# Optimization experiments

Measured on AMD Instinct MI355X. Metric: run time of the kernel, lower is better.

## Reference

```python
import jax, jax.numpy as jnp
import numpy as np

N, D, H, P, B = 6000, 256, 8, 128, 16
DH = D // H


def _layernorm(x, g, b, eps=1e-5):
    mu = jnp.mean(x, axis=-1, keepdims=True)
    var = jnp.mean((x - mu) ** 2, axis=-1, keepdims=True)
    return (x - mu) * jax.lax.rsqrt(var + eps) * g + b


def setup_inputs() -> dict:
    key = jax.random.key(0)
    ks = jax.random.split(key, 12)
    s = 1.0 / np.sqrt(D)
    inp = {
        "H_genes": jax.random.normal(ks[0], (N, D), jnp.float32),
        "perturbation_indices": jax.random.randint(ks[1], (P,), 0, N),
        "batch_assignment": jnp.sort(jax.random.randint(ks[2], (P,), 0, B)),
        "batch_size": B,
        # nn.MultiheadAttention params
        "in_proj_w": jax.random.uniform(ks[3], (3 * D, D), jnp.float32, -s, s),
        "in_proj_b": jnp.zeros((3 * D,), jnp.float32),
        "out_proj_w": jax.random.uniform(ks[4], (D, D), jnp.float32, -s, s),
        "out_proj_b": jnp.zeros((D,), jnp.float32),
        # FFN params
        "ffn_w1": jax.random.uniform(ks[5], (4 * D, D), jnp.float32, -s, s),
        "ffn_b1": jnp.zeros((4 * D,), jnp.float32),
        "ffn_w2": jax.random.uniform(ks[6], (D, 4 * D), jnp.float32, -1.0 / np.sqrt(4 * D), 1.0 / np.sqrt(4 * D)),
        "ffn_b2": jnp.zeros((D,), jnp.float32),
        # LayerNorms
        "ln1_g": jnp.ones((D,), jnp.float32),
        "ln1_b": jnp.zeros((D,), jnp.float32),
        "ln2_g": jnp.ones((D,), jnp.float32),
        "ln2_b": jnp.zeros((D,), jnp.float32),
    }
    return inp


def reference(H_genes, perturbation_indices, batch_assignment, batch_size,
              in_proj_w, in_proj_b, out_proj_w, out_proj_b,
              ffn_w1, ffn_b1, ffn_w2, ffn_b2,
              ln1_g, ln1_b, ln2_g, ln2_b):
    n, d = H_genes.shape
    Wq, Wk, Wv = jnp.split(in_proj_w, 3, axis=0)
    bq, bk, bv = jnp.split(in_proj_b, 3, axis=0)

    # queries: all genes (shared across batch); keys/values: ragged pert context
    q = (H_genes @ Wq.T + bq).reshape(n, H, DH)          # [N,h,dh]
    Hp = H_genes[perturbation_indices]                    # [P,d]
    k = (Hp @ Wk.T + bk).reshape(-1, H, DH)               # [P,h,dh]
    v = (Hp @ Wv.T + bv).reshape(-1, H, DH)               # [P,h,dh]

    scale = 1.0 / np.sqrt(DH)
    scores = jnp.einsum('nhe,phe->hnp', q * scale, k)     # shared scores [h,N,P]

    mask = batch_assignment[None, :] == jnp.arange(batch_size)[:, None]  # [B,P]
    logits = jnp.where(mask[:, None, None, :], scores[None], -1e9)       # [B,h,N,P]
    attn = jax.nn.softmax(logits, axis=-1)

    ctx = jnp.einsum('bhnp,phe->bnhe', attn, v).reshape(batch_size, n, d)
    attn_out = ctx @ out_proj_w.T + out_proj_b            # [B,N,d]

    # torch path: empty perturbation set -> zeros_like attention output
    has_any = mask.any(axis=-1).astype(attn_out.dtype)    # [B]
    attn_out = attn_out * has_any[:, None, None]

    x = _layernorm(H_genes[None] + attn_out, ln1_g, ln1_b)
    ffn = jax.nn.gelu(x @ ffn_w1.T + ffn_b1, approximate=False) @ ffn_w2.T + ffn_b2
    return _layernorm(x + ffn, ln2_g, ln2_b)
```

## Files before the change

### kernel.cpp

```cpp
#include <hip/hip_runtime.h>
#include <math.h>

#define N_GENES 6000
#define DM 256
#define NH 8
#define DHEAD 32
#define FF 1024
#define PMAX 128
#define MT 64
#define LDX 264
#define LDF 260

typedef unsigned short u16;
typedef unsigned int u32;
typedef __attribute__((ext_vector_type(8))) short s8bf;
typedef __attribute__((ext_vector_type(4))) float f4;

__device__ __forceinline__ f4 mfma_bf16(s8bf a, s8bf b, f4 c) {
    return __builtin_amdgcn_mfma_f32_16x16x32_bf16(a, b, c, 0, 0, 0);
}

__device__ __forceinline__ float bf2f(u16 u) { return __uint_as_float(((u32)u) << 16); }
__device__ __forceinline__ u16 f2bf(float f) {
    u32 x = __float_as_uint(f);
    return (u16)((x + 0x7fffu + ((x >> 16) & 1u)) >> 16);
}
__device__ __forceinline__ float gelu_exact(float x) {
    return 0.5f * x * (1.0f + erff(x * 0.70710678118654752f));
}
__device__ __forceinline__ float gelu_fast(float x) {
    float z = fabsf(x) * 0.70710678118654752f;
    float t = 1.0f / (1.0f + 0.3275911f * z);
    float poly = t * (0.254829592f + t * (-0.284496736f + t * (1.421413741f +
                 t * (-1.453152027f + t * 1.061405429f))));
    float erf_abs = 1.0f - poly * __expf(-z * z);
    float erfv = copysignf(erf_abs, x);
    return 0.5f * x * (1.0f + erfv);
}

__global__ __launch_bounds__(256) void prep_kernel(
    const float* __restrict__ Hg, const int* __restrict__ pidx,
    const float* __restrict__ in_w, const float* __restrict__ in_b,
    const float* __restrict__ out_w, const float* __restrict__ w1,
    const float* __restrict__ w2,
    u16* __restrict__ WoP, u16* __restrict__ W1P, u16* __restrict__ W2P,
    float* __restrict__ WqT, float* __restrict__ kbuf, float* __restrict__ vbuf,
    int P) {
    __shared__ float ts[32][33];
    __shared__ float xs[DM];
    int blk = blockIdx.x, tid = threadIdx.x;
    if (blk < 288) {
        const float* src; u16* dst; int K; int c;
        if (blk < 32)       { src = out_w; dst = WoP; K = DM; c = blk * 256 + tid; }
        else if (blk < 160) { src = w1;    dst = W1P; K = DM; c = (blk - 32) * 256 + tid; }
        else                { src = w2;    dst = W2P; K = FF; c = (blk - 160) * 256 + tid; }
        int KT = K >> 5;
        int lane = c & 63;
        int k0i = (c >> 6) % KT;
        int nt = c / (KT << 6);
        const float* s = src + (size_t)(nt * 16 + (lane & 15)) * K + k0i * 32 + (lane >> 4) * 8;
        u16* d = dst + (size_t)c * 8;
        #pragma unroll
        for (int j = 0; j < 8; ++j) d[j] = f2bf(s[j]);
    } else if (blk < 352) {
        int tile = blk - 288;
        int tr = tile >> 3, tc = tile & 7;
        int lane = tid & 31, rowg = tid >> 5;
        #pragma unroll
        for (int i = 0; i < 4; ++i) {
            int r = rowg * 4 + i;
            ts[r][lane] = in_w[(size_t)(tr * 32 + r) * DM + tc * 32 + lane];
        }
        __syncthreads();
        #pragma unroll
        for (int i = 0; i < 4; ++i) {
            int a = rowg * 4 + i;
            WqT[(size_t)(tc * 32 + a) * DM + tr * 32 + lane] = ts[lane][a];
        }
    } else {
        int p = blk - 352;
        if (p >= P) return;
        int d = tid;
        int row = pidx[p];
        xs[d] = Hg[(size_t)row * DM + d];
        __syncthreads();
        const float4* wk = (const float4*)(in_w + (size_t)(DM + d) * DM);
        const float4* wv = (const float4*)(in_w + (size_t)(2 * DM + d) * DM);
        float ak = in_b[DM + d];
        float av = in_b[2 * DM + d];
        #pragma unroll 4
        for (int k = 0; k < DM / 4; ++k) {
            float4 a = wk[k], b = wv[k];
            float x0 = xs[4*k], x1 = xs[4*k+1], x2 = xs[4*k+2], x3 = xs[4*k+3];
            ak += a.x * x0 + a.y * x1 + a.z * x2 + a.w * x3;
            av += b.x * x0 + b.y * x1 + b.z * x2 + b.w * x3;
        }
        kbuf[(size_t)p * DM + d] = ak;
        vbuf[(size_t)p * DM + d] = av;
    }
}

__global__ __launch_bounds__(256) void kvproj_kernel(
    const float* __restrict__ Hg, const int* __restrict__ pidx,
    const float* __restrict__ Win, const float* __restrict__ bin,
    float* __restrict__ kbuf, float* __restrict__ vbuf) {
    __shared__ float xs[DM];
    int p = blockIdx.x, d = threadIdx.x;
    int row = pidx[p];
    xs[d] = Hg[(size_t)row * DM + d];
    __syncthreads();
    const float4* wk = (const float4*)(Win + (size_t)(DM + d) * DM);
    const float4* wv = (const float4*)(Win + (size_t)(2 * DM + d) * DM);
    float ak = bin[DM + d];
    float av = bin[2 * DM + d];
    #pragma unroll 4
    for (int k = 0; k < DM / 4; ++k) {
        float4 a = wk[k], b = wv[k];
        float x0 = xs[4*k], x1 = xs[4*k+1], x2 = xs[4*k+2], x3 = xs[4*k+3];
        ak += a.x * x0 + a.y * x1 + a.z * x2 + a.w * x3;
        av += b.x * x0 + b.y * x1 + b.z * x2 + b.w * x3;
    }
    kbuf[(size_t)p * DM + d] = ak;
    vbuf[(size_t)p * DM + d] = av;
}

__global__ __launch_bounds__(512, 4) void fused_all_kernel(
    const float* __restrict__ Hg, const float* __restrict__ WqT,
    const float* __restrict__ bin,
    const float* __restrict__ kbuf, const float* __restrict__ vbuf,
    const int* __restrict__ assign,
    const u16* __restrict__ WoP, const float* __restrict__ bout,
    const u16* __restrict__ W1P, const float* __restrict__ b1p,
    const u16* __restrict__ W2P, const float* __restrict__ b2p,
    const float* __restrict__ g1, const float* __restrict__ bb1,
    const float* __restrict__ g2, const float* __restrict__ bb2,
    float* __restrict__ out, int P, int B) {

    __shared__ __align__(16) u16 xb[MT][LDX];
    __shared__ __align__(16) char reg2_raw[MT * LDX * 2];
    __shared__ int asg[PMAX];
    __shared__ int startb[16];
    __shared__ int cntb[16];
    __shared__ float hasb[16];

    float* reg2f = (float*)reg2_raw;
    float (*sc)[132] = (float(*)[132])reg2f;
    float* qs   = reg2f + 4224;
    float* hrow = reg2f + 5312;
    float* ps   = reg2f + 6336;
    float (*sb32)[LDF] = (float(*)[LDF])reg2_raw;
    u16  (*hb)[LDX]    = (u16 (*)[LDX])reg2_raw;

    const f4 fzero = {0.f, 0.f, 0.f, 0.f};
    int tid = threadIdx.x;
    int w = tid >> 6, l = tid & 63;
    int l15 = l & 15, q8 = (l >> 4) * 8, q4 = (l >> 4) * 4;
    int n0 = blockIdx.x * 4;

    if (tid < P) asg[tid] = assign[tid];
    for (int i = tid; i < 4 * DM; i += 512)
        hrow[i] = Hg[(size_t)n0 * DM + i];
    __syncthreads();
    if (tid < 16) {
        int s = 0, c = 0;
        for (int p = 0; p < P; ++p) { int a = asg[p]; s += (a < tid); c += (a == tid); }
        startb[tid] = s; cntb[tid] = c; hasb[tid] = c ? 1.f : 0.f;
    }

    {
        int d = tid & 255, kh = tid >> 8;
        const float* wt = WqT + (size_t)(kh * 128) * DM + d;
        float a0 = 0.f, a1 = 0.f, a2 = 0.f, a3 = 0.f;
        const float* h0 = hrow + kh * 128;
        #pragma unroll 8
        for (int k = 0; k < 128; ++k) {
            float wv = wt[(size_t)k * DM];
            a0 += wv * h0[k];
            a1 += wv * h0[256 + k];
            a2 += wv * h0[512 + k];
            a3 += wv * h0[768 + k];
        }
        ps[0 * 512 + kh * 256 + d] = a0;
        ps[1 * 512 + kh * 256 + d] = a1;
        ps[2 * 512 + kh * 256 + d] = a2;
        ps[3 * 512 + kh * 256 + d] = a3;
    }
    __syncthreads();
    for (int i = tid; i < 1024; i += 512) {
        int g = i >> 8, d = i & 255;
        float q = (ps[g * 512 + d] + ps[g * 512 + 256 + d] + bin[d]) * 0.17677669529663687f;
        qs[(g * 8 + (d >> 5)) * 34 + (d & 31)] = q;
    }
    __syncthreads();

    for (int idx = tid; idx < 32 * P; idx += 512) {
        int gh = idx & 31, p = idx >> 5;
        const float* qp = qs + gh * 34;
        const float4* kr = (const float4*)(kbuf + (size_t)p * DM + (gh & 7) * DHEAD);
        float dsum = 0.f;
        #pragma unroll
        for (int e = 0; e < 8; ++e) {
            float4 kv = kr[e];
            dsum += qp[4*e] * kv.x + qp[4*e+1] * kv.y + qp[4*e+2] * kv.z + qp[4*e+3] * kv.w;
        }
        sc[gh][p] = dsum;
    }
    __syncthreads();

    {
        int r = tid >> 3, h = tid & 7;
        int gi = r & 3, bb = r >> 2;
        int s = startb[bb], c = cntb[bb];
        float4 cx[8];
        #pragma unroll
        for (int e = 0; e < 8; ++e) cx[e] = make_float4(0.f, 0.f, 0.f, 0.f);
        if (c > 0) {
            const float* scp = sc[gi * 8 + h];
            float m = -INFINITY;
            for (int i = 0; i < c; ++i) m = fmaxf(m, scp[s + i]);
            float sum = 0.f;
            const float* vb0 = vbuf + h * DHEAD;
            for (int i = 0; i < c; ++i) {
                float wgt = __expf(scp[s + i] - m);
                sum += wgt;
                const float4* vr = (const float4*)(vb0 + (size_t)(s + i) * DM);
                #pragma unroll
                for (int e = 0; e < 8; ++e) {
                    float4 vvv = vr[e];
                    cx[e].x += wgt * vvv.x; cx[e].y += wgt * vvv.y;
                    cx[e].z += wgt * vvv.z; cx[e].w += wgt * vvv.w;
                }
            }
            float inv = 1.0f / sum;
            #pragma unroll
            for (int e = 0; e < 8; ++e) {
                cx[e].x *= inv; cx[e].y *= inv; cx[e].z *= inv; cx[e].w *= inv;
            }
        }
        u16* xrow = &xb[r][h * DHEAD];
        #pragma unroll
        for (int e = 0; e < 8; ++e) {
            *(u32*)(xrow + 4 * e)     = (u32)f2bf(cx[e].x) | ((u32)f2bf(cx[e].y) << 16);
            *(u32*)(xrow + 4 * e + 2) = (u32)f2bf(cx[e].z) | ((u32)f2bf(cx[e].w) << 16);
        }
    }
    __syncthreads();

    f4 acc[4][2] = {fzero, fzero, fzero, fzero, fzero, fzero, fzero, fzero};
    {
        const u16* pb = WoP + (size_t)w * 8192 + (size_t)l * 8;
        s8bf b0 = *(const s8bf*)(pb);
        s8bf b1 = *(const s8bf*)(pb + 4096);
        s8bf a0 = *(const s8bf*)&xb[l15][q8];
        s8bf a1 = *(const s8bf*)&xb[16 + l15][q8];
        s8bf a2 = *(const s8bf*)&xb[32 + l15][q8];
        s8bf a3 = *(const s8bf*)&xb[48 + l15][q8];
        #pragma unroll
        for (int k0i = 0; k0i < 8; ++k0i) {
            s8bf nb0, nb1, na0, na1, na2, na3;
            if (k0i < 7) {
                nb0 = *(const s8bf*)(pb + (k0i + 1) * 512);
                nb1 = *(const s8bf*)(pb + 4096 + (k0i + 1) * 512);
                int k0 = (k0i + 1) * 32 + q8;
                na0 = *(const s8bf*)&xb[l15][k0];
                na1 = *(const s8bf*)&xb[16 + l15][k0];
                na2 = *(const s8bf*)&xb[32 + l15][k0];
                na3 = *(const s8bf*)&xb[48 + l15][k0];
            }
            acc[0][0] = mfma_bf16(a0, b0, acc[0][0]);
            acc[1][0] = mfma_bf16(a1, b0, acc[1][0]);
            acc[2][0] = mfma_bf16(a2, b0, acc[2][0]);
            acc[3][0] = mfma_bf16(a3, b0, acc[3][0]);
            acc[0][1] = mfma_bf16(a0, b1, acc[0][1]);
            acc[1][1] = mfma_bf16(a1, b1, acc[1][1]);
            acc[2][1] = mfma_bf16(a2, b1, acc[2][1]);
            acc[3][1] = mfma_bf16(a3, b1, acc[3][1]);
            if (k0i < 7) { b0 = nb0; b1 = nb1; a0 = na0; a1 = na1; a2 = na2; a3 = na3; }
        }
    }

    auto ln1_pass = [&](int hf, f4 aA0, f4 aA1, f4 aB0, f4 aB1) {
        int cl = w * 32 + l15;
        #pragma unroll
        for (int r = 0; r < 4; ++r) {
            sb32[q4 + r][cl]           = aA0[r];
            sb32[q4 + r][cl + 16]      = aA1[r];
            sb32[16 + q4 + r][cl]      = aB0[r];
            sb32[16 + q4 + r][cl + 16] = aB1[r];
        }
        __syncthreads();
        int r32 = tid >> 4, c4 = (tid & 15) * 4;
        int row = hf * 32 + r32;
        int gi = row & 3, bb = row >> 2;
        float has = hasb[bb];
        const float* hp = Hg + (size_t)(n0 + gi) * DM;
        float tv[16];
        float sum = 0.f;
        #pragma unroll
        for (int jg = 0; jg < 4; ++jg) {
            int c = c4 + jg * 64;
            float4 hv = *(const float4*)(hp + c);
            float4 bv = *(const float4*)(bout + c);
            float t0 = hv.x + has * (sb32[r32][c]     + bv.x);
            float t1 = hv.y + has * (sb32[r32][c + 1] + bv.y);
            float t2 = hv.z + has * (sb32[r32][c + 2] + bv.z);
            float t3 = hv.w + has * (sb32[r32][c + 3] + bv.w);
            tv[jg*4] = t0; tv[jg*4+1] = t1; tv[jg*4+2] = t2; tv[jg*4+3] = t3;
            sum += t0 + t1 + t2 + t3;
        }
        sum += __shfl_xor(sum, 1, 16); sum += __shfl_xor(sum, 2, 16);
        sum += __shfl_xor(sum, 4, 16); sum += __shfl_xor(sum, 8, 16);
        float mu = sum * (1.0f / DM);
        float vs = 0.f;
        #pragma unroll
        for (int j = 0; j < 16; ++j) { float dd = tv[j] - mu; vs += dd * dd; }
        vs += __shfl_xor(vs, 1, 16); vs += __shfl_xor(vs, 2, 16);
        vs += __shfl_xor(vs, 4, 16); vs += __shfl_xor(vs, 8, 16);
        float rs = rsqrtf(vs * (1.0f / DM) + 1e-5f);
        #pragma unroll
        for (int jg = 0; jg < 4; ++jg) {
            int c = c4 + jg * 64;
            float x0 = (tv[jg*4]     - mu) * rs * g1[c]     + bb1[c];
            float x1 = (tv[jg*4 + 1] - mu) * rs * g1[c + 1] + bb1[c + 1];
            float x2 = (tv[jg*4 + 2] - mu) * rs * g1[c + 2] + bb1[c + 2];
            float x3 = (tv[jg*4 + 3] - mu) * rs * g1[c + 3] + bb1[c + 3];
            *(u32*)&xb[row][c]     = (u32)f2bf(x0) | ((u32)f2bf(x1) << 16);
            *(u32*)&xb[row][c + 2] = (u32)f2bf(x2) | ((u32)f2bf(x3) << 16);
        }
        __syncthreads();
    };
    ln1_pass(0, acc[0][0], acc[0][1], acc[1][0], acc[1][1]);
    ln1_pass(1, acc[2][0], acc[2][1], acc[3][0], acc[3][1]);

    f4 acc2[4][2] = {fzero, fzero, fzero, fzero, fzero, fzero, fzero, fzero};
    for (int ch = 0; ch < 4; ++ch) {
        f4 acc1[4][2] = {fzero, fzero, fzero, fzero, fzero, fzero, fzero, fzero};
        {
            const u16* pb = W1P + (size_t)(ch * 16 + 2 * w) * 4096 + (size_t)l * 8;
            s8bf b0 = *(const s8bf*)(pb);
            s8bf b1 = *(const s8bf*)(pb + 4096);
            #pragma unroll
            for (int k0i = 0; k0i < 8; ++k0i) {
                s8bf nb0, nb1;
                if (k0i < 7) {
                    nb0 = *(const s8bf*)(pb + (k0i + 1) * 512);
                    nb1 = *(const s8bf*)(pb + 4096 + (k0i + 1) * 512);
                }
                int k0 = k0i * 32 + q8;
                s8bf a0 = *(const s8bf*)&xb[l15][k0];
                s8bf a1 = *(const s8bf*)&xb[16 + l15][k0];
                s8bf a2 = *(const s8bf*)&xb[32 + l15][k0];
                s8bf a3 = *(const s8bf*)&xb[48 + l15][k0];
                acc1[0][0] = mfma_bf16(a0, b0, acc1[0][0]);
                acc1[1][0] = mfma_bf16(a1, b0, acc1[1][0]);
                acc1[2][0] = mfma_bf16(a2, b0, acc1[2][0]);
                acc1[3][0] = mfma_bf16(a3, b0, acc1[3][0]);
                acc1[0][1] = mfma_bf16(a0, b1, acc1[0][1]);
                acc1[1][1] = mfma_bf16(a1, b1, acc1[1][1]);
                acc1[2][1] = mfma_bf16(a2, b1, acc1[2][1]);
                acc1[3][1] = mfma_bf16(a3, b1, acc1[3][1]);
                if (k0i < 7) { b0 = nb0; b1 = nb1; }
            }
        }
        {
            int cl = w * 32 + l15;
            float bbA = b1p[ch * 256 + cl];
            float bbB = b1p[ch * 256 + cl + 16];
            #pragma unroll
            for (int mt = 0; mt < 4; ++mt)
                #pragma unroll
                for (int r = 0; r < 4; ++r) {
                    hb[mt * 16 + q4 + r][cl]      = f2bf(gelu_fast(acc1[mt][0][r] + bbA));
                    hb[mt * 16 + q4 + r][cl + 16] = f2bf(gelu_fast(acc1[mt][1][r] + bbB));
                }
        }
        __syncthreads();
        {
            const u16* pb = W2P + (size_t)(2 * w) * 16384 + (size_t)(ch * 8) * 512 + (size_t)l * 8;
            s8bf b0 = *(const s8bf*)(pb);
            s8bf b1 = *(const s8bf*)(pb + 16384);
            #pragma unroll
            for (int k0i = 0; k0i < 8; ++k0i) {
                s8bf nb0, nb1;
                if (k0i < 7) {
                    nb0 = *(const s8bf*)(pb + (k0i + 1) * 512);
                    nb1 = *(const s8bf*)(pb + 16384 + (k0i + 1) * 512);
                }
                int k0 = k0i * 32 + q8;
                s8bf a0 = *(const s8bf*)&hb[l15][k0];
                s8bf a1 = *(const s8bf*)&hb[16 + l15][k0];
                s8bf a2 = *(const s8bf*)&hb[32 + l15][k0];
                s8bf a3 = *(const s8bf*)&hb[48 + l15][k0];
                acc2[0][0] = mfma_bf16(a0, b0, acc2[0][0]);
                acc2[1][0] = mfma_bf16(a1, b0, acc2[1][0]);
                acc2[2][0] = mfma_bf16(a2, b0, acc2[2][0]);
                acc2[3][0] = mfma_bf16(a3, b0, acc2[3][0]);
                acc2[0][1] = mfma_bf16(a0, b1, acc2[0][1]);
                acc2[1][1] = mfma_bf16(a1, b1, acc2[1][1]);
                acc2[2][1] = mfma_bf16(a2, b1, acc2[2][1]);
                acc2[3][1] = mfma_bf16(a3, b1, acc2[3][1]);
                if (k0i < 7) { b0 = nb0; b1 = nb1; }
            }
        }
        __syncthreads();
    }

    auto ln2_pass = [&](int hf, f4 aA0, f4 aA1, f4 aB0, f4 aB1) {
        int cl = w * 32 + l15;
        #pragma unroll
        for (int r = 0; r < 4; ++r) {
            sb32[q4 + r][cl]           = aA0[r];
            sb32[q4 + r][cl + 16]      = aA1[r];
            sb32[16 + q4 + r][cl]      = aB0[r];
            sb32[16 + q4 + r][cl + 16] = aB1[r];
        }
        __syncthreads();
        int r32 = tid >> 4, c4 = (tid & 15) * 4;
        int row = hf * 32 + r32;
        int gi = row & 3, bb = row >> 2;
        float tv[16];
        float sum = 0.f;
        #pragma unroll
        for (int jg = 0; jg < 4; ++jg) {
            int c = c4 + jg * 64;
            float4 bv = *(const float4*)(b2p + c);
            float t0 = bf2f(xb[row][c])     + sb32[r32][c]     + bv.x;
            float t1 = bf2f(xb[row][c + 1]) + sb32[r32][c + 1] + bv.y;
            float t2 = bf2f(xb[row][c + 2]) + sb32[r32][c + 2] + bv.z;
            float t3 = bf2f(xb[row][c + 3]) + sb32[r32][c + 3] + bv.w;
            tv[jg*4] = t0; tv[jg*4+1] = t1; tv[jg*4+2] = t2; tv[jg*4+3] = t3;
            sum += t0 + t1 + t2 + t3;
        }
        sum += __shfl_xor(sum, 1, 16); sum += __shfl_xor(sum, 2, 16);
        sum += __shfl_xor(sum, 4, 16); sum += __shfl_xor(sum, 8, 16);
        float mu = sum * (1.0f / DM);
        float vs = 0.f;
        #pragma unroll
        for (int j = 0; j < 16; ++j) { float dd = tv[j] - mu; vs += dd * dd; }
        vs += __shfl_xor(vs, 1, 16); vs += __shfl_xor(vs, 2, 16);
        vs += __shfl_xor(vs, 4, 16); vs += __shfl_xor(vs, 8, 16);
        float rs = rsqrtf(vs * (1.0f / DM) + 1e-5f);
        size_t gr = (size_t)bb * N_GENES + (size_t)(n0 + gi);
        float* op = out + gr * DM;
        #pragma unroll
        for (int jg = 0; jg < 4; ++jg) {
            int c = c4 + jg * 64;
            float4 y;
            y.x = (tv[jg*4]     - mu) * rs * g2[c]     + bb2[c];
            y.y = (tv[jg*4 + 1] - mu) * rs * g2[c + 1] + bb2[c + 1];
            y.z = (tv[jg*4 + 2] - mu) * rs * g2[c + 2] + bb2[c + 2];
            y.w = (tv[jg*4 + 3] - mu) * rs * g2[c + 3] + bb2[c + 3];
            *(float4*)(op + c) = y;
        }
        __syncthreads();
    };
    ln2_pass(0, acc2[0][0], acc2[0][1], acc2[1][0], acc2[1][1]);
    ln2_pass(1, acc2[2][0], acc2[2][1], acc2[3][0], acc2[3][1]);
}

__global__ __launch_bounds__(256) void attn_fb_kernel(
    const float* __restrict__ Hg, const float* __restrict__ kbuf, const float* __restrict__ vbuf,
    const int* __restrict__ assign, const float* __restrict__ Win, const float* __restrict__ bin,
    const float* __restrict__ Wout, const float* __restrict__ bout,
    const float* __restrict__ ln1g, const float* __restrict__ ln1b,
    float* __restrict__ xout, int P) {
    __shared__ float qs[DM];
    __shared__ float hrow[DM];
    __shared__ float sc[NH][PMAX + 1];
    __shared__ float ctxs[DM];
    __shared__ int asg[PMAX];
    __shared__ float red[4];

    int n = blockIdx.x, b = blockIdx.y, tid = threadIdx.x;
    if (tid < P) asg[tid] = assign[tid];
    hrow[tid] = Hg[(size_t)n * DM + tid];
    __syncthreads();
    {
        const float4* wr = (const float4*)(Win + (size_t)tid * DM);
        float acc = bin[tid];
        #pragma unroll 4
        for (int k = 0; k < DM / 4; ++k) {
            float4 w = wr[k];
            acc += w.x * hrow[4*k] + w.y * hrow[4*k+1] + w.z * hrow[4*k+2] + w.w * hrow[4*k+3];
        }
        qs[tid] = acc * 0.17677669529663687f;
        __syncthreads();
    }
    int start = 0, cnt = 0;
    for (int p = 0; p < P; ++p) { int a = asg[p]; start += (a < b); cnt += (a == b); }
    for (int idx = tid; idx < NH * cnt; idx += 256) {
        int h = idx & (NH - 1), pl = idx >> 3;
        const float* krow = kbuf + (size_t)(start + pl) * DM + h * DHEAD;
        const float* qh = qs + h * DHEAD;
        float acc = 0.f;
        #pragma unroll
        for (int e = 0; e < DHEAD; ++e) acc += qh[e] * krow[e];
        sc[h][pl] = acc;
    }
    __syncthreads();
    if (cnt > 0) {
        int h = tid >> 5, ll = tid & 31;
        float m = -INFINITY;
        for (int p = ll; p < cnt; p += 32) m = fmaxf(m, sc[h][p]);
        #pragma unroll
        for (int off = 16; off > 0; off >>= 1) m = fmaxf(m, __shfl_xor(m, off, 32));
        float s = 0.f;
        for (int p = ll; p < cnt; p += 32) { float e = __expf(sc[h][p] - m); sc[h][p] = e; s += e; }
        #pragma unroll
        for (int off = 16; off > 0; off >>= 1) s += __shfl_xor(s, off, 32);
        float inv = 1.0f / s;
        for (int p = ll; p < cnt; p += 32) sc[h][p] *= inv;
    }
    __syncthreads();
    {
        int hh = tid >> 5, e = tid & 31;
        float acc = 0.f;
        for (int p = 0; p < cnt; ++p)
            acc += sc[hh][p] * vbuf[(size_t)(start + p) * DM + hh * DHEAD + e];
        ctxs[tid] = acc;
    }
    __syncthreads();
    float ao = 0.f;
    if (cnt > 0) {
        ao = bout[tid];
        const float4* wr = (const float4*)(Wout + (size_t)tid * DM);
        #pragma unroll 4
        for (int k = 0; k < DM / 4; ++k) {
            float4 w = wr[k];
            ao += w.x * ctxs[4*k] + w.y * ctxs[4*k+1] + w.z * ctxs[4*k+2] + w.w * ctxs[4*k+3];
        }
    }
    float t = hrow[tid] + ao;
    {
        float v = t;
        #pragma unroll
        for (int off = 32; off > 0; off >>= 1) v += __shfl_down(v, off, 64);
        if ((tid & 63) == 0) red[tid >> 6] = v;
        __syncthreads();
        float mu = (red[0] + red[1] + red[2] + red[3]) * (1.0f / DM);
        __syncthreads();
        float dv = t - mu, v2 = dv * dv;
        #pragma unroll
        for (int off = 32; off > 0; off >>= 1) v2 += __shfl_down(v2, off, 64);
        if ((tid & 63) == 0) red[tid >> 6] = v2;
        __syncthreads();
        float var = (red[0] + red[1] + red[2] + red[3]) * (1.0f / DM);
        float xv = dv * rsqrtf(var + 1e-5f) * ln1g[tid] + ln1b[tid];
        xout[((size_t)b * N_GENES + n) * DM + tid] = xv;
    }
}

__global__ __launch_bounds__(256) void ffn_fb_kernel(
    float* __restrict__ xio, const float* __restrict__ W1, const float* __restrict__ b1,
    const float* __restrict__ W2, const float* __restrict__ b2,
    const float* __restrict__ ln2g, const float* __restrict__ ln2b) {
    __shared__ float xs[4][DM];
    __shared__ float hs[4][FF];
    __shared__ float red[4];
    int tid = threadIdx.x;
    size_t row0 = (size_t)blockIdx.x * 4;
    for (int i = tid; i < 4 * DM; i += 256)
        ((float*)xs)[i] = xio[row0 * DM + i];
    __syncthreads();
    for (int oi = 0; oi < FF / 256; ++oi) {
        int o = oi * 256 + tid;
        float bb = b1[o];
        float a0 = bb, a1 = bb, a2 = bb, a3 = bb;
        const float4* wr = (const float4*)(W1 + (size_t)o * DM);
        #pragma unroll 2
        for (int k = 0; k < DM / 4; ++k) {
            float4 w = wr[k];
            a0 += w.x * xs[0][4*k] + w.y * xs[0][4*k+1] + w.z * xs[0][4*k+2] + w.w * xs[0][4*k+3];
            a1 += w.x * xs[1][4*k] + w.y * xs[1][4*k+1] + w.z * xs[1][4*k+2] + w.w * xs[1][4*k+3];
            a2 += w.x * xs[2][4*k] + w.y * xs[2][4*k+1] + w.z * xs[2][4*k+2] + w.w * xs[2][4*k+3];
            a3 += w.x * xs[3][4*k] + w.y * xs[3][4*k+1] + w.z * xs[3][4*k+2] + w.w * xs[3][4*k+3];
        }
        hs[0][o] = gelu_exact(a0); hs[1][o] = gelu_exact(a1);
        hs[2][o] = gelu_exact(a2); hs[3][o] = gelu_exact(a3);
    }
    __syncthreads();
    int d = tid;
    float bb2 = b2[d];
    float c0 = bb2, c1 = bb2, c2 = bb2, c3 = bb2;
    const float4* wr = (const float4*)(W2 + (size_t)d * FF);
    #pragma unroll 2
    for (int k = 0; k < FF / 4; ++k) {
        float4 w = wr[k];
        c0 += w.x * hs[0][4*k] + w.y * hs[0][4*k+1] + w.z * hs[0][4*k+2] + w.w * hs[0][4*k+3];
        c1 += w.x * hs[1][4*k] + w.y * hs[1][4*k+1] + w.z * hs[1][4*k+2] + w.w * hs[1][4*k+3];
        c2 += w.x * hs[2][4*k] + w.y * hs[2][4*k+1] + w.z * hs[2][4*k+2] + w.w * hs[2][4*k+3];
        c3 += w.x * hs[3][4*k] + w.y * hs[3][4*k+1] + w.z * hs[3][4*k+2] + w.w * hs[3][4*k+3];
    }
    float cr[4] = {c0, c1, c2, c3};
    float g = ln2g[d], bln = ln2b[d];
    #pragma unroll
    for (int r = 0; r < 4; ++r) {
        float t = cr[r] + xs[r][d];
        float v = t;
        #pragma unroll
        for (int off = 32; off > 0; off >>= 1) v += __shfl_down(v, off, 64);
        if ((tid & 63) == 0) red[tid >> 6] = v;
        __syncthreads();
        float mu = (red[0] + red[1] + red[2] + red[3]) * (1.0f / DM);
        __syncthreads();
        float dv = t - mu, v2 = dv * dv;
        #pragma unroll
        for (int off = 32; off > 0; off >>= 1) v2 += __shfl_down(v2, off, 64);
        if ((tid & 63) == 0) red[tid >> 6] = v2;
        __syncthreads();
        float var = (red[0] + red[1] + red[2] + red[3]) * (1.0f / DM);
        float y = dv * rsqrtf(var + 1e-5f) * g + bln;
        xio[(row0 + r) * DM + d] = y;
        __syncthreads();
    }
}

extern "C" void kernel_launch(void* const* d_in, const int* in_sizes, int n_in,
                              void* d_out, int out_size, void* d_ws, size_t ws_size,
                              hipStream_t stream) {
    const float* Hg   = (const float*)d_in[0];
    const int* pidx   = (const int*)d_in[1];
    const int* assign = (const int*)d_in[2];
    const float* in_w = (const float*)d_in[4];
    const float* in_b = (const float*)d_in[5];
    const float* out_w= (const float*)d_in[6];
    const float* out_b= (const float*)d_in[7];
    const float* w1   = (const float*)d_in[8];
    const float* b1   = (const float*)d_in[9];
    const float* w2   = (const float*)d_in[10];
    const float* b2   = (const float*)d_in[11];
    const float* g1   = (const float*)d_in[12];
    const float* bb1  = (const float*)d_in[13];
    const float* g2   = (const float*)d_in[14];
    const float* bb2  = (const float*)d_in[15];

    int P = in_sizes[1];
    int B = out_size / (N_GENES * DM);
    size_t nrows = (size_t)B * N_GENES;
    float* out = (float*)d_out;

    size_t woB = (size_t)DM * DM;
    size_t w1B = (size_t)FF * DM;
    size_t w2B = (size_t)DM * FF;
    size_t wqTf = (size_t)DM * DM;
    size_t wbytes = (woB + w1B + w2B) * sizeof(u16) + wqTf * sizeof(float);
    size_t kvbytes = 2 * (size_t)P * DM * sizeof(float);

    if (ws_size >= wbytes + kvbytes && P <= PMAX && B == 16 && (N_GENES % 4) == 0) {
        u16* WoP  = (u16*)d_ws;
        u16* W1P  = WoP + woB;
        u16* W2P  = W1P + w1B;
        float* WqT = (float*)(W2P + w2B);
        float* kbuf = WqT + wqTf;
        float* vbuf = kbuf + (size_t)P * DM;

        prep_kernel<<<352 + P, 256, 0, stream>>>(
            Hg, pidx, in_w, in_b, out_w, w1, w2,
            WoP, W1P, W2P, WqT, kbuf, vbuf, P);
        fused_all_kernel<<<N_GENES / 4, 512, 0, stream>>>(
            Hg, WqT, in_b, kbuf, vbuf, assign,
            WoP, out_b, W1P, b1, W2P, b2, g1, bb1, g2, bb2, out, P, B);
    } else {
        float* kbuf = (float*)d_ws;
        float* vbuf = kbuf + (size_t)P * DM;
        kvproj_kernel<<<P, 256, 0, stream>>>(Hg, pidx, in_w, in_b, kbuf, vbuf);
        attn_fb_kernel<<<dim3(N_GENES, B), 256, 0, stream>>>(
            Hg, kbuf, vbuf, assign, in_w, in_b, out_w, out_b, g1, bb1, out, P);
        ffn_fb_kernel<<<(unsigned)(nrows / 4), 256, 0, stream>>>(
            out, w1, b1, w2, b2, g2, bb2);
    }
}
```

Measured before the change: 484.3 us.

## Shrink shared memory and registers to raise fused kernel occupancy

Reduces LDS footprint by aliasing the score buffer onto the xb tile, narrowing the hidden FFN chunk from 256 to 128 columns, and doing layernorm in 16-row passes instead of 32. Q projection drops the split-K partial-sum buffer and its extra barrier. Register software prefetch in the MFMA loops is removed, and launch bounds are raised from 4 to 6 blocks per CU. The aim is to fit more resident blocks to hide latency. The cost is more barriers, more FFN chunk iterations, and less in-wave load/MFMA overlap.

```diff
diff --git a/kernel.cpp b/kernel.cpp
--- a/kernel.cpp
+++ b/kernel.cpp
@@ -9,7 +9,9 @@
 #define PMAX 128
 #define MT 64
 #define LDX 264
+#define LDH 136
 #define LDF 260
+#define LSC 133
 
 typedef unsigned short u16;
 typedef unsigned int u32;
@@ -124,9 +126,9 @@
     vbuf[(size_t)p * DM + d] = av;
 }
 
-__global__ __launch_bounds__(512, 4) void fused_all_kernel(
-    const float* __restrict__ Hg, const float* __restrict__ WqT,
-    const float* __restrict__ bin,
+__global__ __launch_bounds__(512, 6) void fused_all_kernel(
+    const float* __restrict__ Hg,
+    const float* __restrict__ WqT, const float* __restrict__ bin,
     const float* __restrict__ kbuf, const float* __restrict__ vbuf,
     const int* __restrict__ assign,
     const u16* __restrict__ WoP, const float* __restrict__ bout,
@@ -136,20 +138,20 @@
     const float* __restrict__ g2, const float* __restrict__ bb2,
     float* __restrict__ out, int P, int B) {
 
-    __shared__ __align__(16) u16 xb[MT][LDX];
-    __shared__ __align__(16) char reg2_raw[MT * LDX * 2];
+    __shared__ __align__(16) char xb_raw[MT * LDX * 2];
+    __shared__ __align__(16) char reg2_raw[MT * LDH * 2];
     __shared__ int asg[PMAX];
     __shared__ int startb[16];
     __shared__ int cntb[16];
     __shared__ float hasb[16];
 
+    u16  (*xb)[LDX]  = (u16 (*)[LDX])xb_raw;
+    float (*sc)[LSC] = (float(*)[LSC])xb_raw;
     float* reg2f = (float*)reg2_raw;
-    float (*sc)[132] = (float(*)[132])reg2f;
-    float* qs   = reg2f + 4224;
-    float* hrow = reg2f + 5312;
-    float* ps   = reg2f + 6336;
-    float (*sb32)[LDF] = (float(*)[LDF])reg2_raw;
-    u16  (*hb)[LDX]    = (u16 (*)[LDX])reg2_raw;
+    float* qs   = reg2f;
+    float* hrow = reg2f + 1088;
+    float (*sb16)[LDF] = (float(*)[LDF])reg2_raw;
+    u16  (*hb)[LDH]    = (u16 (*)[LDH])reg2_raw;
 
     const f4 fzero = {0.f, 0.f, 0.f, 0.f};
     int tid = threadIdx.x;
@@ -166,30 +168,22 @@
         for (int p = 0; p < P; ++p) { int a = asg[p]; s += (a < tid); c += (a == tid); }
         startb[tid] = s; cntb[tid] = c; hasb[tid] = c ? 1.f : 0.f;
     }
-
     {
-        int d = tid & 255, kh = tid >> 8;
-        const float* wt = WqT + (size_t)(kh * 128) * DM + d;
-        float a0 = 0.f, a1 = 0.f, a2 = 0.f, a3 = 0.f;
-        const float* h0 = hrow + kh * 128;
+        int d = tid & 255, gp = tid >> 8;
+        const float* wt = WqT + d;
+        const float* hA = hrow + gp * 256;
+        const float* hB = hrow + (gp + 2) * 256;
+        float a0 = 0.f, a1 = 0.f;
         #pragma unroll 8
-        for (int k = 0; k < 128; ++k) {
+        for (int k = 0; k < DM; ++k) {
             float wv = wt[(size_t)k * DM];
-            a0 += wv * h0[k];
-            a1 += wv * h0[256 + k];
-            a2 += wv * h0[512 + k];
-            a3 += wv * h0[768 + k];
-        }
-        ps[0 * 512 + kh * 256 + d] = a0;
-        ps[1 * 512 + kh * 256 + d] = a1;
-        ps[2 * 512 + kh * 256 + d] = a2;
-        ps[3 * 512 + kh * 256 + d] = a3;
-    }
-    __syncthreads();
-    for (int i = tid; i < 1024; i += 512) {
-        int g = i >> 8, d = i & 255;
-        float q = (ps[g * 512 + d] + ps[g * 512 + 256 + d] + bin[d]) * 0.17677669529663687f;
-        qs[(g * 8 + (d >> 5)) * 34 + (d & 31)] = q;
+            a0 += wv * hA[k];
+            a1 += wv * hB[k];
+        }
+        float bq = bin[d];
+        int hsub = (d >> 5) * 34 + (d & 31);
+        qs[(gp * 8) * 34 + hsub]       = (a0 + bq) * 0.17677669529663687f;
+        qs[((gp + 2) * 8) * 34 + hsub] = (a1 + bq) * 0.17677669529663687f;
     }
     __syncthreads();
 
@@ -207,11 +201,11 @@
     }
     __syncthreads();
 
+    float4 cx[8];
     {
         int r = tid >> 3, h = tid & 7;
         int gi = r & 3, bb = r >> 2;
         int s = startb[bb], c = cntb[bb];
-        float4 cx[8];
         #pragma unroll
         for (int e = 0; e < 8; ++e) cx[e] = make_float4(0.f, 0.f, 0.f, 0.f);
         if (c > 0) {
@@ -237,6 +231,10 @@
                 cx[e].x *= inv; cx[e].y *= inv; cx[e].z *= inv; cx[e].w *= inv;
             }
         }
+    }
+    __syncthreads();
+    {
+        int r = tid >> 3, h = tid & 7;
         u16* xrow = &xb[r][h * DHEAD];
         #pragma unroll
         for (int e = 0; e < 8; ++e) {
@@ -249,24 +247,15 @@
     f4 acc[4][2] = {fzero, fzero, fzero, fzero, fzero, fzero, fzero, fzero};
     {
         const u16* pb = WoP + (size_t)w * 8192 + (size_t)l * 8;
-        s8bf b0 = *(const s8bf*)(pb);
-        s8bf b1 = *(const s8bf*)(pb + 4096);
-        s8bf a0 = *(const s8bf*)&xb[l15][q8];
-        s8bf a1 = *(const s8bf*)&xb[16 + l15][q8];
-        s8bf a2 = *(const s8bf*)&xb[32 + l15][q8];
-        s8bf a3 = *(const s8bf*)&xb[48 + l15][q8];
-        #pragma unroll
+        #pragma unroll 4
         for (int k0i = 0; k0i < 8; ++k0i) {
-            s8bf nb0, nb1, na0, na1, na2, na3;
-            if (k0i < 7) {
-                nb0 = *(const s8bf*)(pb + (k0i + 1) * 512);
-                nb1 = *(const s8bf*)(pb + 4096 + (k0i + 1) * 512);
-                int k0 = (k0i + 1) * 32 + q8;
-                na0 = *(const s8bf*)&xb[l15][k0];
-                na1 = *(const s8bf*)&xb[16 + l15][k0];
-                na2 = *(const s8bf*)&xb[32 + l15][k0];
-                na3 = *(const s8bf*)&xb[48 + l15][k0];
-            }
+            s8bf b0 = *(const s8bf*)(pb + k0i * 512);
+            s8bf b1 = *(const s8bf*)(pb + 4096 + k0i * 512);
+            int k0 = k0i * 32 + q8;
+            s8bf a0 = *(const s8bf*)&xb[l15][k0];
+            s8bf a1 = *(const s8bf*)&xb[16 + l15][k0];
+            s8bf a2 = *(const s8bf*)&xb[32 + l15][k0];
+            s8bf a3 = *(const s8bf*)&xb[48 + l15][k0];
             acc[0][0] = mfma_bf16(a0, b0, acc[0][0]);
             acc[1][0] = mfma_bf16(a1, b0, acc[1][0]);
             acc[2][0] = mfma_bf16(a2, b0, acc[2][0]);
@@ -275,117 +264,94 @@
             acc[1][1] = mfma_bf16(a1, b1, acc[1][1]);
             acc[2][1] = mfma_bf16(a2, b1, acc[2][1]);
             acc[3][1] = mfma_bf16(a3, b1, acc[3][1]);
-            if (k0i < 7) { b0 = nb0; b1 = nb1; a0 = na0; a1 = na1; a2 = na2; a3 = na3; }
-        }
-    }
-
-    auto ln1_pass = [&](int hf, f4 aA0, f4 aA1, f4 aB0, f4 aB1) {
+        }
+    }
+
+    auto ln1_pass = [&](int p, f4 aA0, f4 aA1) {
         int cl = w * 32 + l15;
         #pragma unroll
         for (int r = 0; r < 4; ++r) {
-            sb32[q4 + r][cl]           = aA0[r];
-            sb32[q4 + r][cl + 16]      = aA1[r];
-            sb32[16 + q4 + r][cl]      = aB0[r];
-            sb32[16 + q4 + r][cl + 16] = aB1[r];
-        }
-        __syncthreads();
-        int r32 = tid >> 4, c4 = (tid & 15) * 4;
-        int row = hf * 32 + r32;
+            sb16[q4 + r][cl]      = aA0[r];
+            sb16[q4 + r][cl + 16] = aA1[r];
+        }
+        __syncthreads();
+        int r16 = tid >> 5, c8 = (tid & 31) * 8;
+        int row = p * 16 + r16;
         int gi = row & 3, bb = row >> 2;
         float has = hasb[bb];
-        const float* hp = Hg + (size_t)(n0 + gi) * DM;
-        float tv[16];
+        const float* hp = Hg + (size_t)(n0 + gi) * DM + c8;
+        float tv[8];
         float sum = 0.f;
         #pragma unroll
-        for (int jg = 0; jg < 4; ++jg) {
-            int c = c4 + jg * 64;
-            float4 hv = *(const float4*)(hp + c);
-            float4 bv = *(const float4*)(bout + c);
-            float t0 = hv.x + has * (sb32[r32][c]     + bv.x);
-            float t1 = hv.y + has * (sb32[r32][c + 1] + bv.y);
-            float t2 = hv.z + has * (sb32[r32][c + 2] + bv.z);
-            float t3 = hv.w + has * (sb32[r32][c + 3] + bv.w);
-            tv[jg*4] = t0; tv[jg*4+1] = t1; tv[jg*4+2] = t2; tv[jg*4+3] = t3;
+        for (int j = 0; j < 8; j += 4) {
+            float4 hv = *(const float4*)(hp + j);
+            float4 bv = *(const float4*)(bout + c8 + j);
+            float t0 = hv.x + has * (sb16[r16][c8 + j]     + bv.x);
+            float t1 = hv.y + has * (sb16[r16][c8 + j + 1] + bv.y);
+            float t2 = hv.z + has * (sb16[r16][c8 + j + 2] + bv.z);
+            float t3 = hv.w + has * (sb16[r16][c8 + j + 3] + bv.w);
+            tv[j] = t0; tv[j+1] = t1; tv[j+2] = t2; tv[j+3] = t3;
             sum += t0 + t1 + t2 + t3;
         }
-        sum += __shfl_xor(sum, 1, 16); sum += __shfl_xor(sum, 2, 16);
-        sum += __shfl_xor(sum, 4, 16); sum += __shfl_xor(sum, 8, 16);
+        sum += __shfl_xor(sum, 1, 32); sum += __shfl_xor(sum, 2, 32);
+        sum += __shfl_xor(sum, 4, 32); sum += __shfl_xor(sum, 8, 32);
+        sum += __shfl_xor(sum, 16, 32);
         float mu = sum * (1.0f / DM);
         float vs = 0.f;
         #pragma unroll
-        for (int j = 0; j < 16; ++j) { float dd = tv[j] - mu; vs += dd * dd; }
-        vs += __shfl_xor(vs, 1, 16); vs += __shfl_xor(vs, 2, 16);
-        vs += __shfl_xor(vs, 4, 16); vs += __shfl_xor(vs, 8, 16);
+        for (int j = 0; j < 8; ++j) { float dd = tv[j] - mu; vs += dd * dd; }
+        vs += __shfl_xor(vs, 1, 32); vs += __shfl_xor(vs, 2, 32);
+        vs += __shfl_xor(vs, 4, 32); vs += __shfl_xor(vs, 8, 32);
+        vs += __shfl_xor(vs, 16, 32);
         float rs = rsqrtf(vs * (1.0f / DM) + 1e-5f);
         #pragma unroll
-        for (int jg = 0; jg < 4; ++jg) {
-            int c = c4 + jg * 64;
-            float x0 = (tv[jg*4]     - mu) * rs * g1[c]     + bb1[c];
-            float x1 = (tv[jg*4 + 1] - mu) * rs * g1[c + 1] + bb1[c + 1];
-            float x2 = (tv[jg*4 + 2] - mu) * rs * g1[c + 2] + bb1[c + 2];
-            float x3 = (tv[jg*4 + 3] - mu) * rs * g1[c + 3] + bb1[c + 3];
-            *(u32*)&xb[row][c]     = (u32)f2bf(x0) | ((u32)f2bf(x1) << 16);
-            *(u32*)&xb[row][c + 2] = (u32)f2bf(x2) | ((u32)f2bf(x3) << 16);
+        for (int j = 0; j < 8; j += 2) {
+            float x0 = (tv[j]     - mu) * rs * g1[c8 + j]     + bb1[c8 + j];
+            float x1 = (tv[j + 1] - mu) * rs * g1[c8 + j + 1] + bb1[c8 + j + 1];
+            *(u32*)&xb[row][c8 + j] = (u32)f2bf(x0) | ((u32)f2bf(x1) << 16);
         }
         __syncthreads();
     };
-    ln1_pass(0, acc[0][0], acc[0][1], acc[1][0], acc[1][1]);
-    ln1_pass(1, acc[2][0], acc[2][1], acc[3][0], acc[3][1]);
+    ln1_pass(0, acc[0][0], acc[0][1]);
+    ln1_pass(1, acc[1][0], acc[1][1]);
+    ln1_pass(2, acc[2][0], acc[2][1]);
+    ln1_pass(3, acc[3][0], acc[3][1]);
 
     f4 acc2[4][2] = {fzero, fzero, fzero, fzero, fzero, fzero, fzero, fzero};
-    for (int ch = 0; ch < 4; ++ch) {
-        f4 acc1[4][2] = {fzero, fzero, fzero, fzero, fzero, fzero, fzero, fzero};
+    for (int ch = 0; ch < 8; ++ch) {
+        f4 acc1[4] = {fzero, fzero, fzero, fzero};
         {
-            const u16* pb = W1P + (size_t)(ch * 16 + 2 * w) * 4096 + (size_t)l * 8;
-            s8bf b0 = *(const s8bf*)(pb);
-            s8bf b1 = *(const s8bf*)(pb + 4096);
-            #pragma unroll
+            const u16* pb1 = W1P + (size_t)(ch * 8 + w) * 4096 + (size_t)l * 8;
+            #pragma unroll 4
             for (int k0i = 0; k0i < 8; ++k0i) {
-                s8bf nb0, nb1;
-                if (k0i < 7) {
-                    nb0 = *(const s8bf*)(pb + (k0i + 1) * 512);
-                    nb1 = *(const s8bf*)(pb + 4096 + (k0i + 1) * 512);
-                }
+                s8bf b0 = *(const s8bf*)(pb1 + k0i * 512);
                 int k0 = k0i * 32 + q8;
                 s8bf a0 = *(const s8bf*)&xb[l15][k0];
                 s8bf a1 = *(const s8bf*)&xb[16 + l15][k0];
                 s8bf a2 = *(const s8bf*)&xb[32 + l15][k0];
                 s8bf a3 = *(const s8bf*)&xb[48 + l15][k0];
-                acc1[0][0] = mfma_bf16(a0, b0, acc1[0][0]);
-                acc1[1][0] = mfma_bf16(a1, b0, acc1[1][0]);
-                acc1[2][0] = mfma_bf16(a2, b0, acc1[2][0]);
-                acc1[3][0] = mfma_bf16(a3, b0, acc1[3][0]);
-                acc1[0][1] = mfma_bf16(a0, b1, acc1[0][1]);
-                acc1[1][1] = mfma_bf16(a1, b1, acc1[1][1]);
-                acc1[2][1] = mfma_bf16(a2, b1, acc1[2][1]);
-                acc1[3][1] = mfma_bf16(a3, b1, acc1[3][1]);
-                if (k0i < 7) { b0 = nb0; b1 = nb1; }
+                acc1[0] = mfma_bf16(a0, b0, acc1[0]);
+                acc1[1] = mfma_bf16(a1, b0, acc1[1]);
+                acc1[2] = mfma_bf16(a2, b0, acc1[2]);
+                acc1[3] = mfma_bf16(a3, b0, acc1[3]);
             }
         }
         {
-            int cl = w * 32 + l15;
-            float bbA = b1p[ch * 256 + cl];
-            float bbB = b1p[ch * 256 + cl + 16];
+            int cl = w * 16 + l15;
+            float bbA = b1p[ch * 128 + cl];
             #pragma unroll
             for (int mt = 0; mt < 4; ++mt)
                 #pragma unroll
-                for (int r = 0; r < 4; ++r) {
-                    hb[mt * 16 + q4 + r][cl]      = f2bf(gelu_fast(acc1[mt][0][r] + bbA));
-                    hb[mt * 16 + q4 + r][cl + 16] = f2bf(gelu_fast(acc1[mt][1][r] + bbB));
-                }
+                for (int r = 0; r < 4; ++r)
+                    hb[mt * 16 + q4 + r][cl] = f2bf(gelu_fast(acc1[mt][r] + bbA));
         }
         __syncthreads();
         {
-            const u16* pb = W2P + (size_t)(2 * w) * 16384 + (size_t)(ch * 8) * 512 + (size_t)l * 8;
-            s8bf b0 = *(const s8bf*)(pb);
-            s8bf b1 = *(const s8bf*)(pb + 16384);
+            const u16* pb2 = W2P + ((size_t)(2 * w) * 32 + ch * 4) * 512 + (size_t)l * 8;
             #pragma unroll
-            for (int k0i = 0; k0i < 8; ++k0i) {
-                s8bf nb0, nb1;
-                if (k0i < 7) {
-                    nb0 = *(const s8bf*)(pb + (k0i + 1) * 512);
-                    nb1 = *(const s8bf*)(pb + 16384 + (k0i + 1) * 512);
-                }
+            for (int k0i = 0; k0i < 4; ++k0i) {
+                s8bf b0 = *(const s8bf*)(pb2 + k0i * 512);
+                s8bf b1 = *(const s8bf*)(pb2 + 16384 + k0i * 512);
                 int k0 = k0i * 32 + q8;
                 s8bf a0 = *(const s8bf*)&hb[l15][k0];
                 s8bf a1 = *(const s8bf*)&hb[16 + l15][k0];
@@ -399,63 +365,64 @@
                 acc2[1][1] = mfma_bf16(a1, b1, acc2[1][1]);
                 acc2[2][1] = mfma_bf16(a2, b1, acc2[2][1]);
                 acc2[3][1] = mfma_bf16(a3, b1, acc2[3][1]);
-                if (k0i < 7) { b0 = nb0; b1 = nb1; }
             }
         }
         __syncthreads();
     }
 
-    auto ln2_pass = [&](int hf, f4 aA0, f4 aA1, f4 aB0, f4 aB1) {
+    auto ln2_pass = [&](int p, f4 aA0, f4 aA1) {
         int cl = w * 32 + l15;
         #pragma unroll
         for (int r = 0; r < 4; ++r) {
-            sb32[q4 + r][cl]           = aA0[r];
-            sb32[q4 + r][cl + 16]      = aA1[r];
-            sb32[16 + q4 + r][cl]      = aB0[r];
-            sb32[16 + q4 + r][cl + 16] = aB1[r];
-        }
-        __syncthreads();
-        int r32 = tid >> 4, c4 = (tid & 15) * 4;
-        int row = hf * 32 + r32;
+            sb16[q4 + r][cl]      = aA0[r];
+            sb16[q4 + r][cl + 16] = aA1[r];
+        }
+        __syncthreads();
+        int r16 = tid >> 5, c8 = (tid & 31) * 8;
+        int row = p * 16 + r16;
         int gi = row & 3, bb = row >> 2;
-        float tv[16];
+        float tv[8];
         float sum = 0.f;
         #pragma unroll
-        for (int jg = 0; jg < 4; ++jg) {
-            int c = c4 + jg * 64;
-            float4 bv = *(const float4*)(b2p + c);
-            float t0 = bf2f(xb[row][c])     + sb32[r32][c]     + bv.x;
-            float t1 = bf2f(xb[row][c + 1]) + sb32[r32][c + 1] + bv.y;
-            float t2 = bf2f(xb[row][c + 2]) + sb32[r32][c + 2] + bv.z;
-            float t3 = bf2f(xb[row][c + 3]) + sb32[r32][c + 3] + bv.w;
-            tv[jg*4] = t0; tv[jg*4+1] = t1; tv[jg*4+2] = t2; tv[jg*4+3] = t3;
+        for (int j = 0; j < 8; j += 4) {
+            float4 bv = *(const float4*)(b2p + c8 + j);
+            float t0 = bf2f(xb[row][c8 + j])     + sb16[r16][c8 + j]     + bv.x;
+            float t1 = bf2f(xb[row][c8 + j + 1]) + sb16[r16][c8 + j + 1] + bv.y;
+            float t2 = bf2f(xb[row][c8 + j + 2]) + sb16[r16][c8 + j + 2] + bv.z;
+            float t3 = bf2f(xb[row][c8 + j + 3]) + sb16[r16][c8 + j + 3] + bv.w;
+            tv[j] = t0; tv[j+1] = t1; tv[j+2] = t2; tv[j+3] = t3;
             sum += t0 + t1 + t2 + t3;
         }
-        sum += __shfl_xor(sum, 1, 16); sum += __shfl_xor(sum, 2, 16);
-        sum += __shfl_xor(sum, 4, 16); sum += __shfl_xor(sum, 8, 16);
+        sum += __shfl_xor(sum, 1, 32); sum += __shfl_xor(sum, 2, 32);
+        sum += __shfl_xor(sum, 4, 32); sum += __shfl_xor(sum, 8, 32);
+        sum += __shfl_xor(sum, 16, 32);
         float mu = sum * (1.0f / DM);
         float vs = 0.f;
         #pragma unroll
-        for (int j = 0; j < 16; ++j) { float dd = tv[j] - mu; vs += dd * dd; }
-        vs += __shfl_xor(vs, 1, 16); vs += __shfl_xor(vs, 2, 16);
-        vs += __shfl_xor(vs, 4, 16); vs += __shfl_xor(vs, 8, 16);
+        for (int j = 0; j < 8; ++j) { float dd = tv[j] - mu; vs += dd * dd; }
+        vs += __shfl_xor(vs, 1, 32); vs += __shfl_xor(vs, 2, 32);
+        vs += __shfl_xor(vs, 4, 32); vs += __shfl_xor(vs, 8, 32);
+        vs += __shfl_xor(vs, 16, 32);
         float rs = rsqrtf(vs * (1.0f / DM) + 1e-5f);
         size_t gr = (size_t)bb * N_GENES + (size_t)(n0 + gi);
-        float* op = out + gr * DM;
-        #pragma unroll
-        for (int jg = 0; jg < 4; ++jg) {
-            int c = c4 + jg * 64;
-            float4 y;
-            y.x = (tv[jg*4]     - mu) * rs * g2[c]     + bb2[c];
-            y.y = (tv[jg*4 + 1] - mu) * rs * g2[c + 1] + bb2[c + 1];
-            y.z = (tv[jg*4 + 2] - mu) * rs * g2[c + 2] + bb2[c + 2];
-            y.w = (tv[jg*4 + 3] - mu) * rs * g2[c + 3] + bb2[c + 3];
-            *(float4*)(op + c) = y;
-        }
+        float* op = out + gr * DM + c8;
+        float4 y0, y1;
+        y0.x = (tv[0] - mu) * rs * g2[c8 + 0] + bb2[c8 + 0];
+        y0.y = (tv[1] - mu) * rs * g2[c8 + 1] + bb2[c8 + 1];
+        y0.z = (tv[2] - mu) * rs * g2[c8 + 2] + bb2[c8 + 2];
+        y0.w = (tv[3] - mu) * rs * g2[c8 + 3] + bb2[c8 + 3];
+        y1.x = (tv[4] - mu) * rs * g2[c8 + 4] + bb2[c8 + 4];
+        y1.y = (tv[5] - mu) * rs * g2[c8 + 5] + bb2[c8 + 5];
+        y1.z = (tv[6] - mu) * rs * g2[c8 + 6] + bb2[c8 + 6];
+        y1.w = (tv[7] - mu) * rs * g2[c8 + 7] + bb2[c8 + 7];
+        *(float4*)(op) = y0;
+        *(float4*)(op + 4) = y1;
         __syncthreads();
     };
-    ln2_pass(0, acc2[0][0], acc2[0][1], acc2[1][0], acc2[1][1]);
-    ln2_pass(1, acc2[2][0], acc2[2][1], acc2[3][0], acc2[3][1]);
+    ln2_pass(0, acc2[0][0], acc2[0][1]);
+    ln2_pass(1, acc2[1][0], acc2[1][1]);
+    ln2_pass(2, acc2[2][0], acc2[2][1]);
+    ln2_pass(3, acc2[3][0], acc2[3][1]);
 }
 
 __global__ __launch_bounds__(256) void attn_fb_kernel(
@@ -643,10 +610,10 @@
     size_t w1B = (size_t)FF * DM;
     size_t w2B = (size_t)DM * FF;
     size_t wqTf = (size_t)DM * DM;
-    size_t wbytes = (woB + w1B + w2B) * sizeof(u16) + wqTf * sizeof(float);
-    size_t kvbytes = 2 * (size_t)P * DM * sizeof(float);
-
-    if (ws_size >= wbytes + kvbytes && P <= PMAX && B == 16 && (N_GENES % 4) == 0) {
+    size_t kvf  = 2 * (size_t)P * DM;
+    size_t base_bytes = (woB + w1B + w2B) * sizeof(u16) + (wqTf + kvf) * sizeof(float);
+
+    if (ws_size >= base_bytes && P <= PMAX && B == 16 && (N_GENES % 4) == 0) {
         u16* WoP  = (u16*)d_ws;
         u16* W1P  = WoP + woB;
         u16* W2P  = W1P + w1B;
```

After: 647.8 us. 33.8% more time.
